# Performance work log

Measured on AMD Instinct MI355X. Metric: run time of the kernel, lower is better.

Reference implementation:

```python
import jax, jax.numpy as jnp
import numpy as np

B, S, D = 4, 2048, 768
H = 12
HD = D // H  # 64


def setup_inputs() -> dict:
    key = jax.random.key(0)
    k1, k2, k3 = jax.random.split(key, 3)
    scale_qkv = (6.0 / (D + 3 * D)) ** 0.5  # xavier_uniform bound
    scale_o = (6.0 / (D + D)) ** 0.5
    return {
        "x": jax.random.normal(k1, (B, S, D), dtype=jnp.float32),
        "w_qkv": jax.random.uniform(k2, (3 * D, D), dtype=jnp.float32, minval=-scale_qkv, maxval=scale_qkv),
        "b_qkv": jnp.zeros((3 * D,), dtype=jnp.float32),
        "w_o": jax.random.uniform(k3, (D, D), dtype=jnp.float32, minval=-scale_o, maxval=scale_o),
        "b_o": jnp.zeros((D,), dtype=jnp.float32),
    }


def reference(x, w_qkv, b_qkv, w_o, b_o):
    b, s, _ = x.shape
    # qkv projection: [B,S,3D]
    qkv = jnp.einsum("bsd,ed->bse", x, w_qkv) + b_qkv
    # [B,S,H,3*HD] -> [B,H,S,3*HD]
    qkv = qkv.reshape(b, s, H, 3 * HD).transpose(0, 2, 1, 3)
    q, k, v = jnp.split(qkv, 3, axis=-1)  # each [B,H,S,HD]
    # scaled dot-product attention (full score matrix, as in source)
    attn_logits = jnp.einsum("bhqd,bhkd->bhqk", q, k) / np.sqrt(HD).astype(np.float32)
    attention = jax.nn.softmax(attn_logits, axis=-1)
    values = jnp.einsum("bhqk,bhkd->bhqd", attention, v)
    # merge heads: [B,S,D]
    values = values.transpose(0, 2, 1, 3).reshape(b, s, D)
    out = jnp.einsum("bsd,ed->bse", values, w_o) + b_o
    return out
```

## Files before the change

### kernel.cpp

```cpp
#include <hip/hip_runtime.h>
#include <hip/hip_bf16.h>

#define BB 4
#define SS 2048
#define DD 768
#define HH 12
#define HDD 64
#define QKVW 2304

typedef _Float16 h8 __attribute__((ext_vector_type(8)));
typedef _Float16 h2 __attribute__((ext_vector_type(2)));
typedef __fp16 fp16x2 __attribute__((ext_vector_type(2)));
typedef float f4 __attribute__((ext_vector_type(4)));

struct __align__(8) Half4 { _Float16 x, y, z, w; };
struct __align__(8) H2x2 { h2 a, b; };

#define QSCALE 0.18033688011112042f
#define SSHIFT -4.0f

__device__ __forceinline__ h2 pk_cvt(float a, float b) {
    fp16x2 r = __builtin_amdgcn_cvt_pkrtz(a, b);
    return __builtin_bit_cast(h2, r);
}

__global__ __launch_bounds__(256) void cvt16(const float* __restrict__ src,
                                             _Float16* __restrict__ dst, int n4) {
    const int i = blockIdx.x * 256 + threadIdx.x;
    if (i >= n4) return;
    const float4 v = ((const float4*)src)[i];
    Half4 h = {(_Float16)v.x, (_Float16)v.y, (_Float16)v.z, (_Float16)v.w};
    ((Half4*)dst)[i] = h;
}

__device__ __forceinline__ void gload16(const _Float16* g, _Float16* l) {
    __builtin_amdgcn_global_load_lds(
        (const __attribute__((address_space(1))) unsigned int*)g,
        (__attribute__((address_space(3))) unsigned int*)l, 16, 0, 0);
}

template <int EPI>
__global__ __launch_bounds__(256) void gemm_f16(const _Float16* __restrict__ A,
                                                const _Float16* __restrict__ B,
                                                const float* __restrict__ bias,
                                                float* __restrict__ Cf,
                                                _Float16* __restrict__ Ch,
                                                int M, int N, int K) {
    __shared__ _Float16 Ash[2][128 * 32];
    __shared__ _Float16 Bsh[2][128 * 32];

    const int tid = threadIdx.x;
    const int lane = tid & 63;
    const int w = tid >> 6;
    const int l15 = lane & 15;
    const int qd = lane >> 4;
    const int wm = w & 1;
    const int wn = w >> 1;
    const int m0 = blockIdx.y * 128;
    const int n0 = blockIdx.x * 128;
    const int wbase = w * 64;

    f4 acc[4][4];
#pragma unroll
    for (int mt = 0; mt < 4; ++mt)
#pragma unroll
        for (int nt = 0; nt < 4; ++nt) acc[mt][nt] = (f4){0.f, 0.f, 0.f, 0.f};

    const _Float16* Ab = A + (size_t)m0 * K;
    const _Float16* Bb = B + (size_t)n0 * K;

    const int row2 = tid >> 2;
    const int ch8 = (tid & 3) * 8;

    for (int k0 = 0; k0 < K; k0 += 64) {
        __syncthreads();
#pragma unroll
        for (int s = 0; s < 2; ++s) {
#pragma unroll
            for (int i = 0; i < 2; ++i) {
                const size_t gsrc = (size_t)(i * 64 + row2) * K + k0 + s * 32 + ch8;
                const size_t ldst = (size_t)(i * 256 + wbase) * 8;
                gload16(Ab + gsrc, &Ash[s][ldst]);
                gload16(Bb + gsrc, &Bsh[s][ldst]);
            }
        }
        __syncthreads();

#pragma unroll
        for (int s = 0; s < 2; ++s) {
            h8 aF[4], bF[4];
#pragma unroll
            for (int mt = 0; mt < 4; ++mt)
                aF[mt] = *(const h8*)&Ash[s][(wm * 64 + mt * 16 + l15) * 32 + qd * 8];
#pragma unroll
            for (int nt = 0; nt < 4; ++nt)
                bF[nt] = *(const h8*)&Bsh[s][(wn * 64 + nt * 16 + l15) * 32 + qd * 8];
#pragma unroll
            for (int mt = 0; mt < 4; ++mt)
#pragma unroll
                for (int nt = 0; nt < 4; ++nt)
                    acc[mt][nt] = __builtin_amdgcn_mfma_f32_16x16x32_f16(
                        aF[mt], bF[nt], acc[mt][nt], 0, 0, 0);
        }
    }

#pragma unroll
    for (int nt = 0; nt < 4; ++nt) {
        const int n = n0 + wn * 64 + nt * 16 + l15;
        const float bn = bias[n];
        const int qcol = ((n >> 6) % 3) == 0;
#pragma unroll
        for (int mt = 0; mt < 4; ++mt) {
#pragma unroll
            for (int r = 0; r < 4; ++r) {
                const int m = m0 + wm * 64 + mt * 16 + qd * 4 + r;
                float v = acc[mt][nt][r] + bn;
                if (EPI == 0) {
                    Cf[(size_t)m * N + n] = v;
                } else {
                    if (qcol) v *= QSCALE;
                    Ch[(size_t)m * N + n] = (_Float16)v;
                }
            }
        }
    }
}

__global__ __launch_bounds__(256, 3) void attn_mfma(const _Float16* __restrict__ qkvh,
                                                    _Float16* __restrict__ vh) {
    __shared__ _Float16 Kh[64 * 72];
    __shared__ _Float16 VT[64 * 64];
    __shared__ _Float16 Psh[4][32 * 80];

    const int tid = threadIdx.x;
    const int lane = tid & 63;
    const int w = tid >> 6;
    const int l15 = lane & 15;
    const int qd = lane >> 4;
    const int h = blockIdx.y;
    const int b = blockIdx.z;
    const int qbase = blockIdx.x * 128 + w * 32;

    const size_t bhrow = (size_t)b * SS;
    const int hcol = h * 192;

    h8 bQ[2][2];
#pragma unroll
    for (int nt = 0; nt < 2; ++nt)
#pragma unroll
        for (int kc = 0; kc < 2; ++kc)
            bQ[nt][kc] = *(const h8*)(qkvh + (bhrow + qbase + nt * 16 + l15) * QKVW
                                      + hcol + kc * 32 + qd * 8);

    f4 O[4][2];
#pragma unroll
    for (int dt = 0; dt < 4; ++dt)
#pragma unroll
        for (int nt = 0; nt < 2; ++nt) O[dt][nt] = (f4){0.f, 0.f, 0.f, 0.f};
    f4 lacc[2] = {(f4){0.f, 0.f, 0.f, 0.f}, (f4){0.f, 0.f, 0.f, 0.f}};

    h8 ones;
#pragma unroll
    for (int i = 0; i < 8; ++i) ones[i] = (_Float16)1.0f;

    _Float16* Pw = &Psh[w][0];

    const int krow = tid >> 3;
    const int kc8 = (tid & 7) * 8;
    const int vkp = tid & 31;
    const int vc8 = (tid >> 5) * 8;

    h8 kreg[2], vreg[2];
    {
        const _Float16* base = qkvh + (bhrow + 0) * QKVW + hcol;
        kreg[0] = *(const h8*)(base + (size_t)krow * QKVW + 64 + kc8);
        kreg[1] = *(const h8*)(base + (size_t)(32 + krow) * QKVW + 64 + kc8);
        vreg[0] = *(const h8*)(base + (size_t)(2 * vkp) * QKVW + 128 + vc8);
        vreg[1] = *(const h8*)(base + (size_t)(2 * vkp + 1) * QKVW + 128 + vc8);
    }

    for (int kt = 0; kt < SS / 64; ++kt) {
        __syncthreads();
        *(h8*)&Kh[krow * 72 + kc8] = kreg[0];
        *(h8*)&Kh[(32 + krow) * 72 + kc8] = kreg[1];
#pragma unroll
        for (int j = 0; j < 8; ++j) {
            h2 pr = {vreg[0][j], vreg[1][j]};
            *(h2*)&VT[(vc8 + j) * 64 + (((vkp >> 2) ^ j) << 3) + 2 * (vkp & 3)] = pr;
        }
        __syncthreads();

        if (kt + 1 < SS / 64) {
            const _Float16* base = qkvh + (bhrow + (kt + 1) * 64) * QKVW + hcol;
            kreg[0] = *(const h8*)(base + (size_t)krow * QKVW + 64 + kc8);
            kreg[1] = *(const h8*)(base + (size_t)(32 + krow) * QKVW + 64 + kc8);
            vreg[0] = *(const h8*)(base + (size_t)(2 * vkp) * QKVW + 128 + vc8);
            vreg[1] = *(const h8*)(base + (size_t)(2 * vkp + 1) * QKVW + 128 + vc8);
        }

        h8 aK[4][2];
#pragma unroll
        for (int mt = 0; mt < 4; ++mt)
#pragma unroll
            for (int kc = 0; kc < 2; ++kc)
                aK[mt][kc] = *(const h8*)&Kh[(mt * 16 + l15) * 72 + kc * 32 + qd * 8];

#pragma unroll
        for (int mt = 0; mt < 4; ++mt) {
#pragma unroll
            for (int nt = 0; nt < 2; ++nt) {
                f4 z = (f4){SSHIFT, SSHIFT, SSHIFT, SSHIFT};
                z = __builtin_amdgcn_mfma_f32_16x16x32_f16(aK[mt][0], bQ[nt][0], z, 0, 0, 0);
                z = __builtin_amdgcn_mfma_f32_16x16x32_f16(aK[mt][1], bQ[nt][1], z, 0, 0, 0);
                H2x2 pk;
                pk.a = pk_cvt(exp2f(z[0]), exp2f(z[1]));
                pk.b = pk_cvt(exp2f(z[2]), exp2f(z[3]));
                *(H2x2*)&Pw[(nt * 16 + l15) * 80 + mt * 16 + qd * 4] = pk;
            }
        }

        h8 bP[2][2];
#pragma unroll
        for (int nt = 0; nt < 2; ++nt)
#pragma unroll
            for (int kc = 0; kc < 2; ++kc)
                bP[nt][kc] = *(const h8*)&Pw[(nt * 16 + l15) * 80 + kc * 32 + qd * 8];

#pragma unroll
        for (int nt = 0; nt < 2; ++nt) {
            lacc[nt] = __builtin_amdgcn_mfma_f32_16x16x32_f16(ones, bP[nt][0], lacc[nt], 0, 0, 0);
            lacc[nt] = __builtin_amdgcn_mfma_f32_16x16x32_f16(ones, bP[nt][1], lacc[nt], 0, 0, 0);
        }

        h8 aV[4][2];
#pragma unroll
        for (int dt = 0; dt < 4; ++dt)
#pragma unroll
            for (int kc = 0; kc < 2; ++kc) {
                const int d = dt * 16 + l15;
                aV[dt][kc] = *(const h8*)&VT[d * 64 + (((kc * 4 + qd) ^ (d & 7)) << 3)];
            }
#pragma unroll
        for (int dt = 0; dt < 4; ++dt)
#pragma unroll
            for (int nt = 0; nt < 2; ++nt) {
                O[dt][nt] = __builtin_amdgcn_mfma_f32_16x16x32_f16(aV[dt][0], bP[nt][0], O[dt][nt], 0, 0, 0);
                O[dt][nt] = __builtin_amdgcn_mfma_f32_16x16x32_f16(aV[dt][1], bP[nt][1], O[dt][nt], 0, 0, 0);
            }
    }

#pragma unroll
    for (int nt = 0; nt < 2; ++nt) {
        const float linv = 1.0f / lacc[nt][0];
        const size_t row = bhrow + qbase + nt * 16 + l15;
#pragma unroll
        for (int dt = 0; dt < 4; ++dt) {
            f4 o = O[dt][nt];
            Half4 oh;
            oh.x = (_Float16)(o[0] * linv);
            oh.y = (_Float16)(o[1] * linv);
            oh.z = (_Float16)(o[2] * linv);
            oh.w = (_Float16)(o[3] * linv);
            *(Half4*)(vh + row * DD + h * 64 + dt * 16 + qd * 4) = oh;
        }
    }
}

extern "C" void kernel_launch(void* const* d_in, const int* in_sizes, int n_in,
                              void* d_out, int out_size, void* d_ws, size_t ws_size,
                              hipStream_t stream) {
    const float* x     = (const float*)d_in[0];
    const float* w_qkv = (const float*)d_in[1];
    const float* b_qkv = (const float*)d_in[2];
    const float* w_o   = (const float*)d_in[3];
    const float* b_o   = (const float*)d_in[4];
    float* out = (float*)d_out;

    const int M = BB * SS;

    _Float16* p = (_Float16*)d_ws;
    _Float16* qkv_h = p;  p += (size_t)M * QKVW;
    _Float16* xh = p;     p += (size_t)M * DD;
    _Float16* vh = p;     p += (size_t)M * DD;
    _Float16* wqh = p;    p += (size_t)QKVW * DD;
    _Float16* woh = p;    p += (size_t)DD * DD;

    cvt16<<<(M * DD / 4 + 255) / 256, 256, 0, stream>>>(x, xh, M * DD / 4);
    cvt16<<<(QKVW * DD / 4 + 255) / 256, 256, 0, stream>>>(w_qkv, wqh, QKVW * DD / 4);
    cvt16<<<(DD * DD / 4 + 255) / 256, 256, 0, stream>>>(w_o, woh, DD * DD / 4);

    gemm_f16<1><<<dim3(QKVW / 128, M / 128), 256, 0, stream>>>(
        xh, wqh, b_qkv, nullptr, qkv_h, M, QKVW, DD);

    attn_mfma<<<dim3(SS / 128, HH, BB), 256, 0, stream>>>(qkv_h, vh);

    gemm_f16<0><<<dim3(DD / 128, M / 128), 256, 0, stream>>>(
        vh, woh, b_o, out, nullptr, M, DD, DD);
}
```

Measured before the change: 248.9 us.

## Fuse conversion kernels, XOR-swizzle LDS tiles, and vectorize GEMM epilogue

Merges the three fp32-to-fp16 conversion launches into one kernel. Changes the GEMM and attention LDS tiles to an unpadded 64-wide layout with an XOR swizzle so fragment reads avoid bank conflicts, and shrinks the P scratch padding. Swaps the MFMA operand order so each lane holds four consecutive columns, which lets the epilogue do vectorized float4 bias loads and packed 8-byte stores. This trades some index arithmetic and tighter alignment assumptions for fewer launches, fewer LDS conflicts and wider stores.

```diff
diff --git a/kernel.cpp b/kernel.cpp
--- a/kernel.cpp
+++ b/kernel.cpp
@@ -24,10 +24,27 @@
     return __builtin_bit_cast(h2, r);
 }
 
-__global__ __launch_bounds__(256) void cvt16(const float* __restrict__ src,
-                                             _Float16* __restrict__ dst, int n4) {
-    const int i = blockIdx.x * 256 + threadIdx.x;
-    if (i >= n4) return;
+#define N4_X   (BB * SS * DD / 4)
+#define N4_WQ  (QKVW * DD / 4)
+#define N4_WO  (DD * DD / 4)
+#define N4_ALL (N4_X + N4_WQ + N4_WO)
+
+__global__ __launch_bounds__(256) void cvt_all(const float* __restrict__ x,
+                                               const float* __restrict__ wq,
+                                               const float* __restrict__ wo,
+                                               _Float16* __restrict__ xh,
+                                               _Float16* __restrict__ wqh,
+                                               _Float16* __restrict__ woh) {
+    int i = blockIdx.x * 256 + threadIdx.x;
+    const float* src;
+    _Float16* dst;
+    if (i < N4_X) {
+        src = x; dst = xh;
+    } else if (i < N4_X + N4_WQ) {
+        i -= N4_X; src = wq; dst = wqh;
+    } else {
+        i -= N4_X + N4_WQ; src = wo; dst = woh;
+    }
     const float4 v = ((const float4*)src)[i];
     Half4 h = {(_Float16)v.x, (_Float16)v.y, (_Float16)v.z, (_Float16)v.w};
     ((Half4*)dst)[i] = h;
@@ -46,8 +63,8 @@
                                                 float* __restrict__ Cf,
                                                 _Float16* __restrict__ Ch,
                                                 int M, int N, int K) {
-    __shared__ _Float16 Ash[2][128 * 32];
-    __shared__ _Float16 Bsh[2][128 * 32];
+    __shared__ alignas(16) _Float16 Ash[128 * 64];
+    __shared__ alignas(16) _Float16 Bsh[128 * 64];
 
     const int tid = threadIdx.x;
     const int lane = tid & 63;
@@ -58,7 +75,7 @@
     const int wn = w >> 1;
     const int m0 = blockIdx.y * 128;
     const int n0 = blockIdx.x * 128;
-    const int wbase = w * 64;
+    const int ldsb = w * 512;
 
     f4 acc[4][4];
 #pragma unroll
@@ -69,20 +86,17 @@
     const _Float16* Ab = A + (size_t)m0 * K;
     const _Float16* Bb = B + (size_t)n0 * K;
 
-    const int row2 = tid >> 2;
-    const int ch8 = (tid & 3) * 8;
+    const int srow = tid >> 3;
+    const int cg = ((tid & 7) ^ (srow & 7)) * 8;
+    const int x7 = l15 & 7;
 
     for (int k0 = 0; k0 < K; k0 += 64) {
         __syncthreads();
 #pragma unroll
-        for (int s = 0; s < 2; ++s) {
-#pragma unroll
-            for (int i = 0; i < 2; ++i) {
-                const size_t gsrc = (size_t)(i * 64 + row2) * K + k0 + s * 32 + ch8;
-                const size_t ldst = (size_t)(i * 256 + wbase) * 8;
-                gload16(Ab + gsrc, &Ash[s][ldst]);
-                gload16(Bb + gsrc, &Bsh[s][ldst]);
-            }
+        for (int i = 0; i < 4; ++i) {
+            const size_t gsrc = (size_t)(i * 32 + srow) * K + k0 + cg;
+            gload16(Ab + gsrc, Ash + i * 2048 + ldsb);
+            gload16(Bb + gsrc, Bsh + i * 2048 + ldsb);
         }
         __syncthreads();
 
@@ -91,36 +105,40 @@
             h8 aF[4], bF[4];
 #pragma unroll
             for (int mt = 0; mt < 4; ++mt)
-                aF[mt] = *(const h8*)&Ash[s][(wm * 64 + mt * 16 + l15) * 32 + qd * 8];
+                aF[mt] = *(const h8*)&Ash[(wm * 64 + mt * 16 + l15) * 64
+                                          + (((s * 4 + qd) ^ x7) << 3)];
 #pragma unroll
             for (int nt = 0; nt < 4; ++nt)
-                bF[nt] = *(const h8*)&Bsh[s][(wn * 64 + nt * 16 + l15) * 32 + qd * 8];
+                bF[nt] = *(const h8*)&Bsh[(wn * 64 + nt * 16 + l15) * 64
+                                          + (((s * 4 + qd) ^ x7) << 3)];
 #pragma unroll
             for (int mt = 0; mt < 4; ++mt)
 #pragma unroll
                 for (int nt = 0; nt < 4; ++nt)
                     acc[mt][nt] = __builtin_amdgcn_mfma_f32_16x16x32_f16(
-                        aF[mt], bF[nt], acc[mt][nt], 0, 0, 0);
-        }
-    }
-
-#pragma unroll
-    for (int nt = 0; nt < 4; ++nt) {
-        const int n = n0 + wn * 64 + nt * 16 + l15;
-        const float bn = bias[n];
-        const int qcol = ((n >> 6) % 3) == 0;
-#pragma unroll
-        for (int mt = 0; mt < 4; ++mt) {
-#pragma unroll
-            for (int r = 0; r < 4; ++r) {
-                const int m = m0 + wm * 64 + mt * 16 + qd * 4 + r;
-                float v = acc[mt][nt][r] + bn;
-                if (EPI == 0) {
-                    Cf[(size_t)m * N + n] = v;
-                } else {
-                    if (qcol) v *= QSCALE;
-                    Ch[(size_t)m * N + n] = (_Float16)v;
+                        bF[nt], aF[mt], acc[mt][nt], 0, 0, 0);
+        }
+    }
+
+#pragma unroll
+    for (int mt = 0; mt < 4; ++mt) {
+        const int m = m0 + wm * 64 + mt * 16 + l15;
+#pragma unroll
+        for (int nt = 0; nt < 4; ++nt) {
+            const int nb = n0 + wn * 64 + nt * 16 + qd * 4;
+            const float4 bv = *(const float4*)(bias + nb);
+            f4 v = acc[mt][nt];
+            v[0] += bv.x; v[1] += bv.y; v[2] += bv.z; v[3] += bv.w;
+            if (EPI == 0) {
+                *(float4*)(Cf + (size_t)m * N + nb) = (float4){v[0], v[1], v[2], v[3]};
+            } else {
+                if (((nb >> 6) % 3) == 0) {
+                    v[0] *= QSCALE; v[1] *= QSCALE; v[2] *= QSCALE; v[3] *= QSCALE;
                 }
+                H2x2 pk;
+                pk.a = pk_cvt(v[0], v[1]);
+                pk.b = pk_cvt(v[2], v[3]);
+                *(H2x2*)(Ch + (size_t)m * N + nb) = pk;
             }
         }
     }
@@ -128,9 +146,9 @@
 
 __global__ __launch_bounds__(256, 3) void attn_mfma(const _Float16* __restrict__ qkvh,
                                                     _Float16* __restrict__ vh) {
-    __shared__ _Float16 Kh[64 * 72];
-    __shared__ _Float16 VT[64 * 64];
-    __shared__ _Float16 Psh[4][32 * 80];
+    __shared__ alignas(16) _Float16 Kh[64 * 64];
+    __shared__ alignas(16) _Float16 VT[64 * 64];
+    __shared__ alignas(16) _Float16 Psh[4][32 * 72];
 
     const int tid = threadIdx.x;
     const int lane = tid & 63;
@@ -143,6 +161,7 @@
 
     const size_t bhrow = (size_t)b * SS;
     const int hcol = h * 192;
+    const int x7 = l15 & 7;
 
     h8 bQ[2][2];
 #pragma unroll
@@ -167,6 +186,7 @@
 
     const int krow = tid >> 3;
     const int kc8 = (tid & 7) * 8;
+    const int kpc = (((tid & 7) ^ (krow & 7)) << 3);
     const int vkp = tid & 31;
     const int vc8 = (tid >> 5) * 8;
 
@@ -181,8 +201,8 @@
 
     for (int kt = 0; kt < SS / 64; ++kt) {
         __syncthreads();
-        *(h8*)&Kh[krow * 72 + kc8] = kreg[0];
-        *(h8*)&Kh[(32 + krow) * 72 + kc8] = kreg[1];
+        *(h8*)&Kh[krow * 64 + kpc] = kreg[0];
+        *(h8*)&Kh[(32 + krow) * 64 + kpc] = kreg[1];
 #pragma unroll
         for (int j = 0; j < 8; ++j) {
             h2 pr = {vreg[0][j], vreg[1][j]};
@@ -203,7 +223,8 @@
         for (int mt = 0; mt < 4; ++mt)
 #pragma unroll
             for (int kc = 0; kc < 2; ++kc)
-                aK[mt][kc] = *(const h8*)&Kh[(mt * 16 + l15) * 72 + kc * 32 + qd * 8];
+                aK[mt][kc] = *(const h8*)&Kh[(mt * 16 + l15) * 64
+                                             + (((kc * 4 + qd) ^ x7) << 3)];
 
 #pragma unroll
         for (int mt = 0; mt < 4; ++mt) {
@@ -215,7 +236,7 @@
                 H2x2 pk;
                 pk.a = pk_cvt(exp2f(z[0]), exp2f(z[1]));
                 pk.b = pk_cvt(exp2f(z[2]), exp2f(z[3]));
-                *(H2x2*)&Pw[(nt * 16 + l15) * 80 + mt * 16 + qd * 4] = pk;
+                *(H2x2*)&Pw[(nt * 16 + l15) * 72 + mt * 16 + qd * 4] = pk;
             }
         }
 
@@ -224,7 +245,7 @@
         for (int nt = 0; nt < 2; ++nt)
 #pragma unroll
             for (int kc = 0; kc < 2; ++kc)
-                bP[nt][kc] = *(const h8*)&Pw[(nt * 16 + l15) * 80 + kc * 32 + qd * 8];
+                bP[nt][kc] = *(const h8*)&Pw[(nt * 16 + l15) * 72 + kc * 32 + qd * 8];
 
 #pragma unroll
         for (int nt = 0; nt < 2; ++nt) {
@@ -285,9 +306,7 @@
     _Float16* wqh = p;    p += (size_t)QKVW * DD;
     _Float16* woh = p;    p += (size_t)DD * DD;
 
-    cvt16<<<(M * DD / 4 + 255) / 256, 256, 0, stream>>>(x, xh, M * DD / 4);
-    cvt16<<<(QKVW * DD / 4 + 255) / 256, 256, 0, stream>>>(w_qkv, wqh, QKVW * DD / 4);
-    cvt16<<<(DD * DD / 4 + 255) / 256, 256, 0, stream>>>(w_o, woh, DD * DD / 4);
+    cvt_all<<<N4_ALL / 256, 256, 0, stream>>>(x, w_qkv, w_o, xh, wqh, woh);
 
     gemm_f16<1><<<dim3(QKVW / 128, M / 128), 256, 0, stream>>>(
         xh, wqh, b_qkv, nullptr, qkv_h, M, QKVW, DD);
```

Result: no change. 250.2 us (+0.5%).
